# Kernel optimization log

Hardware: AMD Instinct MI355X
Metric: run time of the kernel (lower is better)

## Reference

```python
import jax, jax.numpy as jnp
import numpy as np

N, Q, K, L, H, C, B = 32768, 8192, 16, 8, 128, 20, 4
COS_EPS = 1e-8


def setup_inputs() -> dict:
    key = jax.random.key(0)
    ks = jax.random.split(key, 8)
    support_xyz = jax.random.normal(ks[0], (N, 3), jnp.float32)
    batch_index = jnp.sort(jax.random.randint(ks[1], (N,), 0, B))
    filtered_index = jnp.sort(jax.random.randint(ks[2], (Q,), 0, N))
    gcnfeat = jax.random.normal(ks[3], (N, H + C), jnp.float32)
    leaf_node_all = jax.random.normal(ks[4], (Q, L, 3 * H), jnp.float32)
    W1 = jax.random.normal(ks[5], (10, 64), jnp.float32) * 0.1
    b1 = jnp.zeros((64,), jnp.float32)
    W2 = jax.random.normal(ks[6], (64, H), jnp.float32) * 0.1
    b2 = jnp.zeros((H,), jnp.float32)
    Wl = jax.random.normal(ks[7], (C, H), jnp.float32) * 0.1
    bl = jnp.zeros((H,), jnp.float32)
    return dict(support_xyz=support_xyz, batch_index=batch_index,
                filtered_index=filtered_index, gcnfeat=gcnfeat,
                leaf_node_all=leaf_node_all, W1=W1, b1=b1, W2=W2, b2=b2,
                Wl=Wl, bl=bl)


def _cosine_aff(a, b):
    # a: [Q,L,H], b: [Q,K,H] -> [Q,L,K] cosine similarity matrix
    an = a / jnp.maximum(jnp.linalg.norm(a, axis=-1, keepdims=True), COS_EPS)
    bn = b / jnp.maximum(jnp.linalg.norm(b, axis=-1, keepdims=True), COS_EPS)
    return jnp.einsum('qlh,qkh->qlk', an, bn)


def _auction(mat):
    # Bertsekas auction algorithm (maximization LAP), mat: [L,K], K >= L.
    Lr, Kc = mat.shape
    eps = 1.0 / Lr
    col_ids = jnp.arange(Kc, dtype=jnp.int32)

    def cond(st):
        _, ass = st
        return jnp.any(ass < 0)

    def body(st):
        cost, ass = st
        unassigned = ass < 0                                   # [L]
        value = mat - cost[None, :]                            # [L,K]
        top2, top_idx = jax.lax.top_k(value, 2)
        bid_inc = jnp.where(unassigned, top2[:, 0] - top2[:, 1] + eps, 0.0)
        bids = jnp.zeros((Lr, Kc), mat.dtype).at[jnp.arange(Lr), top_idx[:, 0]].set(bid_inc)
        have_bid = jnp.any(bids > 0, axis=0)                   # [K]
        high_bid = jnp.max(bids, axis=0)                       # [K]
        high_bidder = jnp.argmax(bids, axis=0).astype(jnp.int32)
        cost = cost + jnp.where(have_bid, high_bid, 0.0)
        # kick out previous owners of columns that received bids
        kicked = (ass >= 0) & have_bid[jnp.clip(ass, 0, Kc - 1)]
        ass = jnp.where(kicked, -1, ass)
        # assign the high bidder of each bid-receiving column (others dropped OOB)
        tgt = jnp.where(have_bid, high_bidder, Lr)
        ass = ass.at[tgt].set(col_ids, mode='drop')
        return cost, ass

    cost0 = jnp.zeros((Kc,), mat.dtype)
    ass0 = jnp.full((Lr,), -1, jnp.int32)
    _, ass = jax.lax.while_loop(cond, body, (cost0, ass0))
    return ass


def reference(support_xyz, batch_index, filtered_index, gcnfeat, leaf_node_all,
              W1, b1, W2, b2, Wl, bl):
    query_xyz = support_xyz[filtered_index]                    # [Q,3]
    qb = batch_index[filtered_index]                           # [Q]
    # batched KNN: squared distances via GEMM form, mask cross-batch pairs
    d2 = (jnp.sum(query_xyz ** 2, -1)[:, None]
          + jnp.sum(support_xyz ** 2, -1)[None, :]
          - 2.0 * query_xyz @ support_xyz.T)                   # [Q,N]
    d2 = jnp.where(qb[:, None] == batch_index[None, :], d2, jnp.inf)
    _, col = jax.lax.top_k(-d2, K)                             # [Q,K]
    xyz_j = support_xyz[col]                                   # [Q,K,3]
    xyz_i = jnp.broadcast_to(query_xyz[:, None, :], xyz_j.shape)
    diff = xyz_i - xyz_j
    dist = jnp.linalg.norm(diff, axis=-1, keepdims=True)
    ew = jnp.concatenate([xyz_i, xyz_j, diff, dist], axis=-1)  # [Q,K,10]
    edge_w = jax.nn.relu(ew @ W1 + b1) @ W2 + b2               # [Q,K,H] rel_map
    feat_j = gcnfeat[col]                                      # [Q,K,H+C]
    cls_w = feat_j[..., -C:] @ Wl + bl                         # [Q,K,H] label_map
    m1 = _cosine_aff(leaf_node_all[:, :, :H], edge_w)
    m2 = _cosine_aff(leaf_node_all[:, :, H:2 * H], cls_w)
    m3 = _cosine_aff(leaf_node_all[:, :, 2 * H:], feat_j[..., :H])
    mat = (m1 + m2) / 4.0 + m3 / 2.0                           # [Q,L,K]
    gm_idx = jax.vmap(_auction)(jax.lax.stop_gradient(mat))    # [Q,L]
    scores = jnp.take_along_axis(mat, gm_idx[:, :, None].astype(jnp.int32), axis=2)[..., 0]
    return jnp.mean(scores, axis=-1)                           # [Q]
```

## Files before the change

### kernel.cpp

```cpp
#include <hip/hip_runtime.h>
#include <stdint.h>

#define KNN 16
#define LROWS 8
#define KBQ 8
#define KCAP 128

__device__ __forceinline__ void load4(const float* __restrict__ sxyz, int i0,
                                      int N, float px[4], float py[4],
                                      float pz[4]) {
  if (i0 + 4 <= N) {
    float4 v0 = *(const float4*)&sxyz[3 * i0];
    float4 v1 = *(const float4*)&sxyz[3 * i0 + 4];
    float4 v2 = *(const float4*)&sxyz[3 * i0 + 8];
    px[0] = v0.x; py[0] = v0.y; pz[0] = v0.z;
    px[1] = v0.w; py[1] = v1.x; pz[1] = v1.y;
    px[2] = v1.z; py[2] = v1.w; pz[2] = v2.x;
    px[3] = v2.y; py[3] = v2.z; pz[3] = v2.w;
  } else {
#pragma unroll
    for (int e = 0; e < 4; ++e) {
      int i = i0 + e; bool ok = i < N;
      px[e] = ok ? sxyz[3 * i] : 0.f;
      py[e] = ok ? sxyz[3 * i + 1] : 0.f;
      pz[e] = ok ? sxyz[3 * i + 2] : 0.f;
    }
  }
}

__global__ __launch_bounds__(256) void knn_kernel(
    const float* __restrict__ sxyz, const int* __restrict__ bidx,
    const int* __restrict__ fidx, int* __restrict__ col, int N, int Q) {
  const int t = threadIdx.x;
  const int qbase = blockIdx.x * KBQ;

  __shared__ float s_min[KBQ][256];
  __shared__ unsigned long long s_cand[KBQ][KCAP];
  __shared__ int s_cnt[KBQ];
  __shared__ float s_thr[KBQ];
  __shared__ float s_qx[KBQ], s_qy[KBQ], s_qz[KBQ];
  __shared__ int s_lo[KBQ], s_hi[KBQ];

  if (t < 2 * KBQ) {
    int qi = qbase + (t & (KBQ - 1));
    if (qi < Q) {
      int fi = fidx[qi];
      int qb = bidx[fi];
      if (t < KBQ) {
        s_qx[t] = sxyz[3 * fi]; s_qy[t] = sxyz[3 * fi + 1]; s_qz[t] = sxyz[3 * fi + 2];
        int a = 0, b = N;
        while (a < b) { int m = (a + b) >> 1; if (bidx[m] < qb) a = m + 1; else b = m; }
        s_lo[t] = a;
      } else {
        int a = 0, b = N;
        while (a < b) { int m = (a + b) >> 1; if (bidx[m] <= qb) a = m + 1; else b = m; }
        s_hi[t - KBQ] = a;
      }
    } else {
      if (t < KBQ) { s_lo[t] = 0; s_qx[t] = s_qy[t] = s_qz[t] = 0.f; }
      else s_hi[t - KBQ] = 0;
    }
  }
  if (t < KBQ) s_cnt[t] = 0;
  __syncthreads();

  float qx[KBQ], qy[KBQ], qz[KBQ], qmin[KBQ];
  int qlo[KBQ], qhi[KBQ];
#pragma unroll
  for (int qi = 0; qi < KBQ; ++qi) {
    qx[qi] = s_qx[qi]; qy[qi] = s_qy[qi]; qz[qi] = s_qz[qi];
    qlo[qi] = s_lo[qi]; qhi[qi] = s_hi[qi];
    qmin[qi] = 3e38f;
  }
  int blo = qlo[0], bhi = qhi[0];
#pragma unroll
  for (int qi = 1; qi < KBQ; ++qi) { blo = min(blo, qlo[qi]); bhi = max(bhi, qhi[qi]); }
  const int base = blo & ~3;

  for (int i0 = base + 4 * t; i0 < bhi; i0 += 1024) {
    float px[4], py[4], pz[4];
    load4(sxyz, i0, N, px, py, pz);
#pragma unroll
    for (int e = 0; e < 4; ++e) {
      int i = i0 + e;
#pragma unroll
      for (int qi = 0; qi < KBQ; ++qi) {
        float dx = qx[qi] - px[e], dy = qy[qi] - py[e], dz = qz[qi] - pz[e];
        float d2 = fmaf(dx, dx, fmaf(dy, dy, dz * dz));
        bool v = (i >= qlo[qi]) && (i < qhi[qi]);
        qmin[qi] = fminf(qmin[qi], v ? d2 : 3e38f);
      }
    }
  }
#pragma unroll
  for (int qi = 0; qi < KBQ; ++qi) s_min[qi][t] = qmin[qi];
  __syncthreads();

  {
    int qi = t >> 5, u = t & 31;
    float v[8];
#pragma unroll
    for (int s = 0; s < 8; ++s) v[s] = s_min[qi][u + 32 * s];
    float thr = 3e38f;
    for (int r = 0; r < KNN; ++r) {
      float lm = fminf(fminf(fminf(v[0], v[1]), fminf(v[2], v[3])),
                       fminf(fminf(v[4], v[5]), fminf(v[6], v[7])));
      float gm = lm;
      gm = fminf(gm, __shfl_xor(gm, 1, 64));
      gm = fminf(gm, __shfl_xor(gm, 2, 64));
      gm = fminf(gm, __shfl_xor(gm, 4, 64));
      gm = fminf(gm, __shfl_xor(gm, 8, 64));
      gm = fminf(gm, __shfl_xor(gm, 16, 64));
      unsigned long long b = __ballot(lm == gm);
      unsigned mask = (unsigned)((b >> (t & 32)) & 0xffffffffull);
      int win = __ffs(mask) - 1;
      if (u == win) {
        if (v[0] == gm) v[0] = 3e38f; else if (v[1] == gm) v[1] = 3e38f;
        else if (v[2] == gm) v[2] = 3e38f; else if (v[3] == gm) v[3] = 3e38f;
        else if (v[4] == gm) v[4] = 3e38f; else if (v[5] == gm) v[5] = 3e38f;
        else if (v[6] == gm) v[6] = 3e38f; else v[7] = 3e38f;
      }
      thr = gm;
    }
    if (u == 0)
      s_thr[qi] = (s_hi[qi] - s_lo[qi] <= KCAP) ? 3e38f : thr;
  }
  __syncthreads();

  float qthr[KBQ];
#pragma unroll
  for (int qi = 0; qi < KBQ; ++qi) qthr[qi] = s_thr[qi];

  for (int i0 = base + 4 * t; i0 < bhi; i0 += 1024) {
    float px[4], py[4], pz[4];
    load4(sxyz, i0, N, px, py, pz);
#pragma unroll
    for (int e = 0; e < 4; ++e) {
      int i = i0 + e;
#pragma unroll
      for (int qi = 0; qi < KBQ; ++qi) {
        float dx = qx[qi] - px[e], dy = qy[qi] - py[e], dz = qz[qi] - pz[e];
        float d2 = fmaf(dx, dx, fmaf(dy, dy, dz * dz));
        if (i >= qlo[qi] && i < qhi[qi] && d2 <= qthr[qi]) {
          int pos = atomicAdd(&s_cnt[qi], 1);
          if (pos < KCAP)
            s_cand[qi][pos] =
                (((unsigned long long)__float_as_uint(d2)) << 32) | (unsigned)i;
        }
      }
    }
  }
  __syncthreads();

  {
    int qi = t >> 5, u = t & 31;
    int M = min(s_cnt[qi], KCAP);
    for (int r = 0; r < KNN; ++r) {
      unsigned long long lm = ~0ull; int ls = -1;
      for (int s = u; s < M; s += 32) {
        unsigned long long vv = s_cand[qi][s];
        if (vv < lm) { lm = vv; ls = s; }
      }
      unsigned long long gm = lm, o;
      o = __shfl_xor(gm, 1, 64); if (o < gm) gm = o;
      o = __shfl_xor(gm, 2, 64); if (o < gm) gm = o;
      o = __shfl_xor(gm, 4, 64); if (o < gm) gm = o;
      o = __shfl_xor(gm, 8, 64); if (o < gm) gm = o;
      o = __shfl_xor(gm, 16, 64); if (o < gm) gm = o;
      unsigned long long b = __ballot(lm == gm);
      unsigned mask = (unsigned)((b >> (t & 32)) & 0xffffffffull);
      int win = __ffs(mask) - 1;
      if (u == win && ls >= 0 && gm != ~0ull) {
        s_cand[qi][ls] = ~0ull;
        col[(size_t)(qbase + qi) * KNN + r] = (int)(unsigned)(gm & 0xffffffffull);
      }
    }
  }
}

#define OFF_EDGE 0
#define OFF_B 2080
#define OFF_EW 4160
#define OFF_FC 4352
#define S_TOTAL 4672

template <bool EXT>
__global__ __launch_bounds__(256) void fused_kernel(
    const float* __restrict__ sxyz,
    const int* __restrict__ fidx,
    const float* __restrict__ gcn,
    const float* __restrict__ leaf,
    const float* __restrict__ W1, const float* __restrict__ b1,
    const float* __restrict__ W2, const float* __restrict__ b2,
    const float* __restrict__ Wl, const float* __restrict__ bl,
    const int* __restrict__ col,
    float* __restrict__ matw, float* __restrict__ out) {
  const int q = blockIdx.x;
  const int t = threadIdx.x;
  const int h = t & 127;
  const int kh = (t >> 7) * 8;

  __shared__ __align__(16) float S[S_TOTAL];
  __shared__ int s_col[KNN];
  __shared__ float s_rna[24];
  __shared__ float s_rnb[3][KNN];

  const float* lq = leaf + (size_t)q * 3072;

  if (t < KNN) s_col[t] = col[q * KNN + t];
  __syncthreads();

  for (int v = t; v < KNN * 20; v += 256)
    S[OFF_FC + v] = gcn[(size_t)s_col[v / 20] * 148 + 128 + (v % 20)];
  if (t < KNN) {
    int fi = fidx[q];
    float qx = sxyz[3 * fi], qy = sxyz[3 * fi + 1], qz = sxyz[3 * fi + 2];
    int j = s_col[t];
    float jx = sxyz[3 * j], jy = sxyz[3 * j + 1], jz = sxyz[3 * j + 2];
    float dx = qx - jx, dy = qy - jy, dz = qz - jz;
    float dist = sqrtf(dx * dx + dy * dy + dz * dz);
    float* e = &S[OFF_EW + t * 12];
    e[0] = qx; e[1] = qy; e[2] = qz;
    e[3] = jx; e[4] = jy; e[5] = jz;
    e[6] = dx; e[7] = dy; e[8] = dz; e[9] = dist;
  }
  __syncthreads();

  for (int r = 0; r < 4; ++r) {
    int o = r * 256 + t;
    int k = o >> 6, jj = o & 63;
    float acc0 = b1[jj];
#pragma unroll
    for (int i = 0; i < 10; ++i)
      acc0 = fmaf(S[OFF_EW + k * 12 + i], W1[i * 64 + jj], acc0);
    S[OFF_B + k * 68 + jj] = fmaxf(acc0, 0.0f);
  }
  __syncthreads();

  float acc[8];
#pragma unroll
  for (int k = 0; k < 8; ++k) acc[k] = b2[h];
#pragma unroll
  for (int j4 = 0; j4 < 16; ++j4) {
    float w0 = W2[(4 * j4 + 0) * 128 + h];
    float w1 = W2[(4 * j4 + 1) * 128 + h];
    float w2 = W2[(4 * j4 + 2) * 128 + h];
    float w3 = W2[(4 * j4 + 3) * 128 + h];
#pragma unroll
    for (int k = 0; k < 8; ++k) {
      float4 hv = *(const float4*)&S[OFF_B + (kh + k) * 68 + 4 * j4];
      acc[k] = fmaf(hv.x, w0, acc[k]);
      acc[k] = fmaf(hv.y, w1, acc[k]);
      acc[k] = fmaf(hv.z, w2, acc[k]);
      acc[k] = fmaf(hv.w, w3, acc[k]);
    }
  }
#pragma unroll
  for (int k = 0; k < 8; ++k) S[OFF_EDGE + (kh + k) * 130 + h] = acc[k];
  __syncthreads();

#pragma unroll
  for (int k = 0; k < 8; ++k) acc[k] = bl[h];
#pragma unroll
  for (int c = 0; c < 20; ++c) {
    float wv = Wl[c * 128 + h];
#pragma unroll
    for (int k = 0; k < 8; ++k)
      acc[k] = fmaf(S[OFF_FC + (kh + k) * 20 + c], wv, acc[k]);
  }
#pragma unroll
  for (int k = 0; k < 8; ++k) S[OFF_B + (kh + k) * 130 + h] = acc[k];
  __syncthreads();

  if (t < 72) {
    float s0 = 0, s1 = 0, s2 = 0, s3 = 0;
    if (t < 24 || t >= 56) {
      const float4* p = (t < 24)
          ? (const float4*)(lq + (t / 3) * 384 + (t % 3) * 128)
          : (const float4*)(gcn + (size_t)s_col[t - 56] * 148);
#pragma unroll 4
      for (int hh = 0; hh < 32; ++hh) {
        float4 v = p[hh];
        s0 = fmaf(v.x, v.x, s0); s1 = fmaf(v.y, v.y, s1);
        s2 = fmaf(v.z, v.z, s2); s3 = fmaf(v.w, v.w, s3);
      }
    } else {
      const float* p = (t < 40) ? &S[OFF_EDGE + (t - 24) * 130]
                                : &S[OFF_B + (t - 40) * 130];
#pragma unroll 4
      for (int hh = 0; hh < 128; hh += 4) {
        float2 v0 = *(const float2*)&p[hh];
        float2 v1 = *(const float2*)&p[hh + 2];
        s0 = fmaf(v0.x, v0.x, s0); s1 = fmaf(v0.y, v0.y, s1);
        s2 = fmaf(v1.x, v1.x, s2); s3 = fmaf(v1.y, v1.y, s3);
      }
    }
    float rn = 1.0f / fmaxf(sqrtf((s0 + s1) + (s2 + s3)), 1e-8f);
    if (t < 24) s_rna[t] = rn;
    else if (t < 40) s_rnb[0][t - 24] = rn;
    else if (t < 56) s_rnb[1][t - 40] = rn;
    else s_rnb[2][t - 56] = rn;
  }
  __syncthreads();

  if (t < 128) {
    int l = t >> 4, k = t & 15;
    const float* a0 = lq + l * 384;
    const float* be = &S[OFF_EDGE + k * 130];
    const float* bc = &S[OFF_B + k * 130];
    const float* bf = gcn + (size_t)s_col[k] * 148;
    float d0 = 0, d1 = 0, d2 = 0;
    for (int hh = 0; hh < 128; hh += 4) {
      float4 va0 = *(const float4*)&a0[hh];
      float4 va1 = *(const float4*)&a0[128 + hh];
      float4 va2 = *(const float4*)&a0[256 + hh];
      float4 vbf = *(const float4*)&bf[hh];
      float2 ve0 = *(const float2*)&be[hh];
      float2 ve1 = *(const float2*)&be[hh + 2];
      float2 vc0 = *(const float2*)&bc[hh];
      float2 vc1 = *(const float2*)&bc[hh + 2];
      d0 = fmaf(va0.x, ve0.x, d0); d0 = fmaf(va0.y, ve0.y, d0);
      d0 = fmaf(va0.z, ve1.x, d0); d0 = fmaf(va0.w, ve1.y, d0);
      d1 = fmaf(va1.x, vc0.x, d1); d1 = fmaf(va1.y, vc0.y, d1);
      d1 = fmaf(va1.z, vc1.x, d1); d1 = fmaf(va1.w, vc1.y, d1);
      d2 = fmaf(va2.x, vbf.x, d2); d2 = fmaf(va2.y, vbf.y, d2);
      d2 = fmaf(va2.z, vbf.z, d2); d2 = fmaf(va2.w, vbf.w, d2);
    }
    float m = (d0 * s_rna[l * 3 + 0] * s_rnb[0][k] +
               d1 * s_rna[l * 3 + 1] * s_rnb[1][k]) * 0.25f +
              d2 * s_rna[l * 3 + 2] * s_rnb[2][k] * 0.5f;
    if (EXT) matw[(size_t)q * 128 + t] = m;
    else S[OFF_EW + l * 17 + k] = m;
  }
  if (EXT) return;
  __syncthreads();
  if (t >= 64) return;

  const float* s_mat = &S[OFF_EW];
  float mrow[KNN];
#pragma unroll
  for (int c = 0; c < KNN; ++c) mrow[c] = s_mat[(t & 7) * 17 + c];
  int ass = -1;
  float cost = 0.f;
  for (int it = 0; it < 1024; ++it) {
    float v1 = -3e38f, v2 = -3e38f; int c1 = 0;
#pragma unroll
    for (int c = 0; c < KNN; ++c) {
      float costc = __shfl(cost, c, 64);
      float v = mrow[c] - costc;
      if (v > v1) { v2 = v1; v1 = v; c1 = c; }
      else if (v > v2) v2 = v;
    }
    int bidc = (t < 8 && ass < 0) ? c1 : -1;
    float bidv = v1 - v2 + 0.125f;
    float high = -3e38f; int hb = -1;
#pragma unroll
    for (int r = 0; r < 8; ++r) {
      int bc = __shfl(bidc, r, 64);
      float bv = __shfl(bidv, r, 64);
      if (bc == t && bv > high) { high = bv; hb = r; }
    }
    if (t < 16 && hb >= 0) cost += high;
    int hb_c = __shfl(hb, bidc < 0 ? 0 : bidc, 64);
    int hb_a = __shfl(hb, ass < 0 ? 0 : ass, 64);
    if (t < 8) {
      if (ass >= 0 && hb_a >= 0) ass = -1;
      if (bidc >= 0 && hb_c == t) ass = bidc;
    }
    if (__ballot((t < 8) ? (ass >= 0) : 1) == ~0ull) break;
  }
  float s = 0.f;
#pragma unroll
  for (int r = 0; r < 8; ++r) {
    int a = __shfl(ass, r, 64);
    if (t == 0) s += s_mat[r * 17 + a];
  }
  if (t == 0) out[q] = s * 0.125f;
}

__global__ __launch_bounds__(256) void auction_kernel(
    const float* __restrict__ matw, float* __restrict__ out, int Q) {
  const int t = threadIdx.x;
  const int lane = t & 63;
  const int gj = lane & 15;
  const int gb = lane & ~15;
  const int q = blockIdx.x * 16 + (t >> 6) * 4 + (lane >> 4);
  const bool valid = q < Q;

  float mrow[KNN];
  if (valid && gj < 8) {
    const float4* mp = (const float4*)(matw + (size_t)q * 128 + gj * 16);
    float4 a = mp[0], b = mp[1], c = mp[2], d = mp[3];
    mrow[0] = a.x; mrow[1] = a.y; mrow[2] = a.z; mrow[3] = a.w;
    mrow[4] = b.x; mrow[5] = b.y; mrow[6] = b.z; mrow[7] = b.w;
    mrow[8] = c.x; mrow[9] = c.y; mrow[10] = c.z; mrow[11] = c.w;
    mrow[12] = d.x; mrow[13] = d.y; mrow[14] = d.z; mrow[15] = d.w;
  } else {
#pragma unroll
    for (int c = 0; c < KNN; ++c) mrow[c] = 0.f;
  }
  int ass = (valid && gj < 8) ? -1 : 0;
  float cost = 0.f;

  for (int it = 0; it < 512; ++it) {
    float v1 = -3e38f, v2 = -3e38f; int c1 = 0;
#pragma unroll
    for (int c = 0; c < KNN; ++c) {
      float costc = __shfl(cost, gb + c, 64);
      float v = mrow[c] - costc;
      if (v > v1) { v2 = v1; v1 = v; c1 = c; }
      else if (v > v2) v2 = v;
    }
    int bidc = (valid && gj < 8 && ass < 0) ? c1 : -1;
    float bidv = v1 - v2 + 0.125f;

    float high = -3e38f; int hb = -1;
#pragma unroll
    for (int r = 0; r < 8; ++r) {
      int bc = __shfl(bidc, gb + r, 64);
      float bv = __shfl(bidv, gb + r, 64);
      if (bc == gj && bv > high) { high = bv; hb = r; }
    }
    if (hb >= 0) cost += high;

    int hb_c = __shfl(hb, gb + (bidc < 0 ? 0 : bidc), 64);
    int hb_a = __shfl(hb, gb + (ass < 0 ? 0 : ass), 64);
    if (valid && gj < 8) {
      if (ass >= 0 && hb_a >= 0) ass = -1;
      if (bidc >= 0 && hb_c == gj) ass = bidc;
    }
    if (__ballot(ass >= 0) == ~0ull) break;
  }

  float val = 0.f;
  if (valid && gj < 8) {
#pragma unroll
    for (int c = 0; c < KNN; ++c) val = (ass == c) ? mrow[c] : val;
  }
  val += __shfl_xor(val, 1, 64);
  val += __shfl_xor(val, 2, 64);
  val += __shfl_xor(val, 4, 64);
  if (valid && gj == 0) out[q] = val * 0.125f;
}

extern "C" void kernel_launch(void* const* d_in, const int* in_sizes, int n_in,
                              void* d_out, int out_size, void* d_ws, size_t ws_size,
                              hipStream_t stream) {
  const float* sxyz = (const float*)d_in[0];
  const int* bidx = (const int*)d_in[1];
  const int* fidx = (const int*)d_in[2];
  const float* gcn = (const float*)d_in[3];
  const float* leaf = (const float*)d_in[4];
  const float* W1 = (const float*)d_in[5];
  const float* b1 = (const float*)d_in[6];
  const float* W2 = (const float*)d_in[7];
  const float* b2 = (const float*)d_in[8];
  const float* Wl = (const float*)d_in[9];
  const float* bl = (const float*)d_in[10];
  float* out = (float*)d_out;

  const int N = in_sizes[0] / 3;
  const int Q = in_sizes[2];

  char* ws = (char*)d_ws;
  int* col = (int*)ws;
  float* matw = (float*)(ws + (size_t)Q * KNN * 4);
  const size_t need = (size_t)Q * KNN * 4 + (size_t)Q * 128 * 4;

  knn_kernel<<<(Q + KBQ - 1) / KBQ, 256, 0, stream>>>(sxyz, bidx, fidx, col, N, Q);
  if (ws_size >= need) {
    fused_kernel<true><<<Q, 256, 0, stream>>>(sxyz, fidx, gcn, leaf, W1, b1, W2,
                                              b2, Wl, bl, col, matw, out);
    auction_kernel<<<(Q + 15) / 16, 256, 0, stream>>>(matw, out, Q);
  } else {
    fused_kernel<false><<<Q, 256, 0, stream>>>(sxyz, fidx, gcn, leaf, W1, b1, W2,
                                               b2, Wl, bl, col, nullptr, out);
  }
}
```

Baseline: 398.8 us.

## Remap W2 matmul threads to vectorized weight loads and pad LDS rows to 132

```diff
diff --git a/kernel.cpp b/kernel.cpp
--- a/kernel.cpp
+++ b/kernel.cpp
@@ -179,10 +179,10 @@
 }
 
 #define OFF_EDGE 0
-#define OFF_B 2080
-#define OFF_EW 4160
-#define OFF_FC 4352
-#define S_TOTAL 4672
+#define OFF_B 2112
+#define OFF_EW 4224
+#define OFF_FC 4416
+#define S_TOTAL 4736
 
 template <bool EXT>
 __global__ __launch_bounds__(256) void fused_kernel(
@@ -237,39 +237,56 @@
   }
   __syncthreads();
 
-  float acc[8];
-#pragma unroll
-  for (int k = 0; k < 8; ++k) acc[k] = b2[h];
-#pragma unroll
-  for (int j4 = 0; j4 < 16; ++j4) {
-    float w0 = W2[(4 * j4 + 0) * 128 + h];
-    float w1 = W2[(4 * j4 + 1) * 128 + h];
-    float w2 = W2[(4 * j4 + 2) * 128 + h];
-    float w3 = W2[(4 * j4 + 3) * 128 + h];
+  {
+    const int k2 = t & 15, hb = (t >> 4) * 8;
+    float a0 = b2[hb + 0], a1 = b2[hb + 1], a2 = b2[hb + 2], a3 = b2[hb + 3];
+    float a4 = b2[hb + 4], a5 = b2[hb + 5], a6 = b2[hb + 6], a7 = b2[hb + 7];
+#pragma unroll
+    for (int j4 = 0; j4 < 16; ++j4) {
+      float4 hv = *(const float4*)&S[OFF_B + k2 * 68 + 4 * j4];
+      const float* w2r = &W2[(4 * j4) * 128 + hb];
+#pragma unroll
+      for (int jj = 0; jj < 4; ++jj) {
+        float hvj = (jj == 0) ? hv.x : (jj == 1) ? hv.y : (jj == 2) ? hv.z : hv.w;
+        float4 wa = *(const float4*)&w2r[jj * 128];
+        float4 wb = *(const float4*)&w2r[jj * 128 + 4];
+        a0 = fmaf(hvj, wa.x, a0); a1 = fmaf(hvj, wa.y, a1);
+        a2 = fmaf(hvj, wa.z, a2); a3 = fmaf(hvj, wa.w, a3);
+        a4 = fmaf(hvj, wb.x, a4); a5 = fmaf(hvj, wb.y, a5);
+        a6 = fmaf(hvj, wb.z, a6); a7 = fmaf(hvj, wb.w, a7);
+      }
+    }
+    *(float4*)&S[OFF_EDGE + k2 * 132 + hb] = make_float4(a0, a1, a2, a3);
+    *(float4*)&S[OFF_EDGE + k2 * 132 + hb + 4] = make_float4(a4, a5, a6, a7);
+  }
+  __syncthreads();
+
+  {
+    float wl[20];
+#pragma unroll
+    for (int c = 0; c < 20; ++c) wl[c] = Wl[c * 128 + h];
 #pragma unroll
     for (int k = 0; k < 8; ++k) {
-      float4 hv = *(const float4*)&S[OFF_B + (kh + k) * 68 + 4 * j4];
-      acc[k] = fmaf(hv.x, w0, acc[k]);
-      acc[k] = fmaf(hv.y, w1, acc[k]);
-      acc[k] = fmaf(hv.z, w2, acc[k]);
-      acc[k] = fmaf(hv.w, w3, acc[k]);
-    }
-  }
-#pragma unroll
-  for (int k = 0; k < 8; ++k) S[OFF_EDGE + (kh + k) * 130 + h] = acc[k];
-  __syncthreads();
-
-#pragma unroll
-  for (int k = 0; k < 8; ++k) acc[k] = bl[h];
-#pragma unroll
-  for (int c = 0; c < 20; ++c) {
-    float wv = Wl[c * 128 + h];
-#pragma unroll
-    for (int k = 0; k < 8; ++k)
-      acc[k] = fmaf(S[OFF_FC + (kh + k) * 20 + c], wv, acc[k]);
-  }
-#pragma unroll
-  for (int k = 0; k < 8; ++k) S[OFF_B + (kh + k) * 130 + h] = acc[k];
+      const float* fc = &S[OFF_FC + (kh + k) * 20];
+      float4 f0 = *(const float4*)&fc[0];
+      float4 f1 = *(const float4*)&fc[4];
+      float4 f2 = *(const float4*)&fc[8];
+      float4 f3 = *(const float4*)&fc[12];
+      float4 f4 = *(const float4*)&fc[16];
+      float a = bl[h];
+      a = fmaf(f0.x, wl[0], a);  a = fmaf(f0.y, wl[1], a);
+      a = fmaf(f0.z, wl[2], a);  a = fmaf(f0.w, wl[3], a);
+      a = fmaf(f1.x, wl[4], a);  a = fmaf(f1.y, wl[5], a);
+      a = fmaf(f1.z, wl[6], a);  a = fmaf(f1.w, wl[7], a);
+      a = fmaf(f2.x, wl[8], a);  a = fmaf(f2.y, wl[9], a);
+      a = fmaf(f2.z, wl[10], a); a = fmaf(f2.w, wl[11], a);
+      a = fmaf(f3.x, wl[12], a); a = fmaf(f3.y, wl[13], a);
+      a = fmaf(f3.z, wl[14], a); a = fmaf(f3.w, wl[15], a);
+      a = fmaf(f4.x, wl[16], a); a = fmaf(f4.y, wl[17], a);
+      a = fmaf(f4.z, wl[18], a); a = fmaf(f4.w, wl[19], a);
+      S[OFF_B + (kh + k) * 132 + h] = a;
+    }
+  }
   __syncthreads();
 
   if (t < 72) {
@@ -285,8 +302,8 @@
         s2 = fmaf(v.z, v.z, s2); s3 = fmaf(v.w, v.w, s3);
       }
     } else {
-      const float* p = (t < 40) ? &S[OFF_EDGE + (t - 24) * 130]
-                                : &S[OFF_B + (t - 40) * 130];
+      const float* p = (t < 40) ? &S[OFF_EDGE + (t - 24) * 132]
+                                : &S[OFF_B + (t - 40) * 132];
 #pragma unroll 4
       for (int hh = 0; hh < 128; hh += 4) {
         float2 v0 = *(const float2*)&p[hh];
@@ -305,24 +322,22 @@
 
   if (t < 128) {
     int l = t >> 4, k = t & 15;
-    const float* a0 = lq + l * 384;
-    const float* be = &S[OFF_EDGE + k * 130];
-    const float* bc = &S[OFF_B + k * 130];
+    const float* a0p = lq + l * 384;
+    const float* be = &S[OFF_EDGE + k * 132];
+    const float* bc = &S[OFF_B + k * 132];
     const float* bf = gcn + (size_t)s_col[k] * 148;
     float d0 = 0, d1 = 0, d2 = 0;
     for (int hh = 0; hh < 128; hh += 4) {
-      float4 va0 = *(const float4*)&a0[hh];
-      float4 va1 = *(const float4*)&a0[128 + hh];
-      float4 va2 = *(const float4*)&a0[256 + hh];
+      float4 va0 = *(const float4*)&a0p[hh];
+      float4 va1 = *(const float4*)&a0p[128 + hh];
+      float4 va2 = *(const float4*)&a0p[256 + hh];
       float4 vbf = *(const float4*)&bf[hh];
-      float2 ve0 = *(const float2*)&be[hh];
-      float2 ve1 = *(const float2*)&be[hh + 2];
-      float2 vc0 = *(const float2*)&bc[hh];
-      float2 vc1 = *(const float2*)&bc[hh + 2];
-      d0 = fmaf(va0.x, ve0.x, d0); d0 = fmaf(va0.y, ve0.y, d0);
-      d0 = fmaf(va0.z, ve1.x, d0); d0 = fmaf(va0.w, ve1.y, d0);
-      d1 = fmaf(va1.x, vc0.x, d1); d1 = fmaf(va1.y, vc0.y, d1);
-      d1 = fmaf(va1.z, vc1.x, d1); d1 = fmaf(va1.w, vc1.y, d1);
+      float4 ve = *(const float4*)&be[hh];
+      float4 vc = *(const float4*)&bc[hh];
+      d0 = fmaf(va0.x, ve.x, d0); d0 = fmaf(va0.y, ve.y, d0);
+      d0 = fmaf(va0.z, ve.z, d0); d0 = fmaf(va0.w, ve.w, d0);
+      d1 = fmaf(va1.x, vc.x, d1); d1 = fmaf(va1.y, vc.y, d1);
+      d1 = fmaf(va1.z, vc.z, d1); d1 = fmaf(va1.w, vc.w, d1);
       d2 = fmaf(va2.x, vbf.x, d2); d2 = fmaf(va2.y, vbf.y, d2);
       d2 = fmaf(va2.z, vbf.z, d2); d2 = fmaf(va2.w, vbf.w, d2);
     }
```

New measurement: 486.4 us. 1.22x slower.
